# Kernel tuning notes

Hardware: AMD Instinct MI355X
Metric: run time of the kernel (lower is better)

The kernel has to match this reference:

```python
import jax, jax.numpy as jnp
import numpy as np

NEG_INF = -1e10  # masked_fill value from the torch module


def setup_inputs() -> dict:
    key = jax.random.key(0)
    k1, k2, k3, k4, k5 = jax.random.split(key, 5)
    B, S, H = 64, 2048, 512
    return {
        "decoder_hidden": jax.random.normal(k1, (B, H), dtype=jnp.float32),
        "encoder_outputs": jax.random.normal(k2, (B, S, 2 * H), dtype=jnp.float32),
        "mask": jnp.ones((B, S), dtype=jnp.int32),
        "Wd": jax.random.normal(k3, (H, H), dtype=jnp.float32) * (1.0 / np.sqrt(H)),
        "We": jax.random.normal(k4, (2 * H, H), dtype=jnp.float32) * (1.0 / np.sqrt(2 * H)),
        "v": jax.random.normal(k5, (H,), dtype=jnp.float32) * (1.0 / np.sqrt(H)),
    }


def reference(decoder_hidden, encoder_outputs, mask, Wd, We, v):
    # decoder_proj: (B, H); encoder_proj: (B, S, H)
    dec_proj = decoder_hidden @ Wd
    enc_proj = jnp.einsum("bse,eh->bsh", encoder_outputs, We)
    energy = jnp.tanh(dec_proj[:, None, :] + enc_proj)  # (B, S, H)
    scores = jnp.einsum("bsh,h->bs", energy, v)  # (B, S)
    scores = jnp.where(mask == 0, NEG_INF, scores)
    attn_weights = jax.nn.softmax(scores, axis=1)  # (B, S)
    context = jnp.einsum("bs,bsd->bd", attn_weights, encoder_outputs)  # (B, 2H)
    return (context, attn_weights)
```

## Files before the change

### kernel.cpp

```cpp
#include <hip/hip_runtime.h>

typedef _Float16 f16;
typedef f16  f16x4 __attribute__((ext_vector_type(4)));
typedef f16  f16x8 __attribute__((ext_vector_type(8)));
typedef float f32x4 __attribute__((ext_vector_type(4)));

#define B_  64
#define S_  2048
#define H_  512
#define K_  1024

__device__ __forceinline__ float fast_tanh(float x){
  float ax = fabsf(x);
  float t  = __expf(-2.0f*ax);
  float r  = (1.0f - t) / (1.0f + t);
  return x < 0.0f ? -r : r;
}

__global__ __launch_bounds__(256) void convert_we_k(const float* __restrict__ We,
                                                    f16* __restrict__ Bg){
  int idx = blockIdx.x*256 + threadIdx.x;
  int k = idx >> 9, col = idx & 511;
  Bg[((k>>3)<<12) + (col<<3) + (k&7)] = (f16)We[idx];
}

__global__ __launch_bounds__(128) void decproj_k(const float* __restrict__ dh,
                                                 const float* __restrict__ Wd,
                                                 float* __restrict__ dp){
  __shared__ float s_dh[512];
  int b = blockIdx.x >> 2, cg = blockIdx.x & 3;
  int col = (cg<<7) + threadIdx.x;
  for (int i = threadIdx.x; i < 512; i += 128) s_dh[i] = dh[(b<<9) + i];
  __syncthreads();
  float a0=0.f,a1=0.f,a2=0.f,a3=0.f;
  for (int k = 0; k < 512; k += 4){
    a0 += s_dh[k+0]*Wd[(k+0)*512 + col];
    a1 += s_dh[k+1]*Wd[(k+1)*512 + col];
    a2 += s_dh[k+2]*Wd[(k+2)*512 + col];
    a3 += s_dh[k+3]*Wd[(k+3)*512 + col];
  }
  dp[(b<<9) + col] = (a0+a1)+(a2+a3);
}

__global__ __launch_bounds__(512, 4) void scores_k(
    const float* __restrict__ enc,
    const f16*   __restrict__ Bg,
    const float* __restrict__ dp,
    const float* __restrict__ vvg,
    float*       __restrict__ scores)
{
  __shared__ __align__(16) f16 At[2][2048];
  __shared__ __align__(16) f16 Bt[2][16384];
  __shared__ float s_sc[64];

  const int tid  = threadIdx.x;
  const int lane = tid & 63;
  const int wave = tid >> 6;
  const int b    = blockIdx.x >> 5;
  const int s0   = (blockIdx.x & 31) << 6;

  if (tid < 64) s_sc[tid] = 0.0f;

  const int arow = tid >> 3;
  const int akq  = tid & 7;
  const float* aG = enc + ((size_t)(b*S_ + s0 + arow) << 10) + (akq << 2);
  const int aDst = ((akq>>1)<<9) + (arow<<3) + ((akq&1)<<2);

  const int r16 = lane & 15, g = lane >> 4;
  const int aFrag = (g<<9)  + (r16<<3);
  const int colb  = wave << 6;
  const int bFrag = (g<<12) + ((colb + r16)<<3);

  f32x4 acc[4][4] = {};

  auto stage = [&](int buf, int t){
    const f16* src = Bg + ((size_t)t << 14);
    #pragma unroll
    for (int i = 0; i < 4; ++i){
      int slot = (i<<9) + tid;
      __builtin_amdgcn_global_load_lds(
          (const __attribute__((address_space(1))) void*)(src + (slot<<3)),
          (__attribute__((address_space(3))) void*)(&Bt[buf][slot<<3]),
          16, 0, 0);
    }
    f32x4 a4 = __builtin_nontemporal_load((const f32x4*)(aG + (t<<5)));
    f16x4 h4; h4[0]=(f16)a4[0]; h4[1]=(f16)a4[1]; h4[2]=(f16)a4[2]; h4[3]=(f16)a4[3];
    *(f16x4*)&At[buf][aDst] = h4;
  };

  stage(0, 0);
  __syncthreads();

  for (int t = 0; t < 32; ++t){
    const int cur = t & 1;
    if (t < 31) stage(cur^1, t+1);
    f16x8 bfr[4];
    #pragma unroll
    for (int n = 0; n < 4; ++n) bfr[n] = *(const f16x8*)&Bt[cur][bFrag + (n<<7)];
    #pragma unroll
    for (int m = 0; m < 4; ++m){
      f16x8 af = *(const f16x8*)&At[cur][aFrag + (m<<7)];
      #pragma unroll
      for (int n = 0; n < 4; ++n)
        acc[m][n] = __builtin_amdgcn_mfma_f32_16x16x32_f16(af, bfr[n], acc[m][n], 0, 0, 0);
    }
    __syncthreads();
  }

  float dpv[4], vvv[4];
  #pragma unroll
  for (int n = 0; n < 4; ++n){
    int c = colb + (n<<4) + r16;
    dpv[n] = dp[(b<<9) + c];
    vvv[n] = vvg[c];
  }
  float sp[4][4] = {};
  #pragma unroll
  for (int m = 0; m < 4; ++m)
    #pragma unroll
    for (int n = 0; n < 4; ++n)
      #pragma unroll
      for (int r = 0; r < 4; ++r){
        float e = fast_tanh(acc[m][n][r] + dpv[n]);
        sp[m][r] += vvv[n]*e;
      }
  #pragma unroll
  for (int m = 0; m < 4; ++m)
    #pragma unroll
    for (int r = 0; r < 4; ++r){
      float x = sp[m][r];
      x += __shfl_xor(x, 1);
      x += __shfl_xor(x, 2);
      x += __shfl_xor(x, 4);
      x += __shfl_xor(x, 8);
      if (r16 == 0) atomicAdd(&s_sc[(m<<4) + (g<<2) + r], x);
    }
  __syncthreads();
  if (tid < 64) scores[((size_t)b << 11) + s0 + tid] = s_sc[tid];
}

__global__ __launch_bounds__(256) void softmax_k(const float* __restrict__ sc,
                                                 const int* __restrict__ mask,
                                                 float* __restrict__ attn){
  const int b = blockIdx.x, tid = threadIdx.x;
  const int lane = tid & 63, wv = tid >> 6;
  __shared__ float rmx[4], rsm[4];
  float vals[8];
  float mx = -3.0e38f;
  #pragma unroll
  for (int i = 0; i < 8; ++i){
    int s = tid + (i<<8);
    float x = sc[(b<<11) + s];
    if (mask[(b<<11) + s] == 0) x = -1e10f;
    vals[i] = x; mx = fmaxf(mx, x);
  }
  #pragma unroll
  for (int o = 32; o >= 1; o >>= 1) mx = fmaxf(mx, __shfl_xor(mx, o));
  if (lane == 0) rmx[wv] = mx;
  __syncthreads();
  mx = fmaxf(fmaxf(rmx[0],rmx[1]), fmaxf(rmx[2],rmx[3]));
  float sm = 0.f;
  #pragma unroll
  for (int i = 0; i < 8; ++i){ vals[i] = __expf(vals[i]-mx); sm += vals[i]; }
  #pragma unroll
  for (int o = 32; o >= 1; o >>= 1) sm += __shfl_xor(sm, o);
  if (lane == 0) rsm[wv] = sm;
  __syncthreads();
  sm = rsm[0]+rsm[1]+rsm[2]+rsm[3];
  float inv = 1.0f / sm;
  #pragma unroll
  for (int i = 0; i < 8; ++i) attn[(b<<11) + tid + (i<<8)] = vals[i]*inv;
}

__global__ __launch_bounds__(256) void ctx_partial_k(const float* __restrict__ enc,
                                                     const float* __restrict__ attn,
                                                     float* __restrict__ part){
  const int b = blockIdx.x >> 4, ch = blockIdx.x & 15;
  const int tid = threadIdx.x;
  const f32x4* e4 = (const f32x4*)(enc + ((size_t)(b*S_ + (ch<<7)) << 10)) + tid;
  const float* aw = attn + (b<<11) + (ch<<7);
  f32x4 acc = {0.f,0.f,0.f,0.f};
  #pragma unroll 4
  for (int s = 0; s < 128; ++s){
    float w = aw[s];
    f32x4 x = __builtin_nontemporal_load(e4 + s*256);
    acc += w * x;
  }
  ((f32x4*)part)[(blockIdx.x<<8) + tid] = acc;
}

__global__ __launch_bounds__(256) void ctx_reduce_k(const float* __restrict__ part,
                                                    float* __restrict__ ctx){
  const int b = blockIdx.x, tid = threadIdx.x;
  f32x4 acc = {0.f,0.f,0.f,0.f};
  #pragma unroll
  for (int c = 0; c < 16; ++c)
    acc += ((const f32x4*)part)[(((b<<4)+c)<<8) + tid];
  ((f32x4*)ctx)[(b<<8) + tid] = acc;
}

extern "C" void kernel_launch(void* const* d_in, const int* in_sizes, int n_in,
                              void* d_out, int out_size, void* d_ws, size_t ws_size,
                              hipStream_t stream){
  (void)in_sizes; (void)n_in; (void)out_size;
  const size_t WS_NEED = (1u<<20) + B_*H_*4 + B_*S_*4 + (4u<<20);
  if (ws_size < WS_NEED) return;

  const float* dec_h = (const float*)d_in[0];
  const float* enc   = (const float*)d_in[1];
  const int*   mask  = (const int*)d_in[2];
  const float* Wd    = (const float*)d_in[3];
  const float* We    = (const float*)d_in[4];
  const float* v     = (const float*)d_in[5];
  float* out  = (float*)d_out;
  float* ctx  = out;
  float* attn = out + B_*2*H_;

  f16*   Bg     = (f16*)d_ws;
  float* dproj  = (float*)((char*)d_ws + (1<<20));
  float* scores = dproj + B_*H_;
  float* part   = scores + B_*S_;

  convert_we_k <<<2048, 256, 0, stream>>>(We, Bg);
  decproj_k    <<<256, 128, 0, stream>>>(dec_h, Wd, dproj);
  scores_k     <<<2048, 512, 0, stream>>>(enc, Bg, dproj, v, scores);
  softmax_k    <<<B_, 256, 0, stream>>>(scores, mask, attn);
  ctx_partial_k<<<B_*16, 256, 0, stream>>>(enc, attn, part);
  ctx_reduce_k <<<B_, 256, 0, stream>>>(part, ctx);
}
```

Measured before the change: 323.3 us.

## Double scores tile rows, merge prep kernels, fuse softmax into context pass

The scores GEMM tile grows from 64 to 128 sequence rows per block, which halves how often the We tile is re-read per encoder row. The cost is twice the accumulators and lower occupancy (launch bounds 4 to 2). The We conversion and decoder projection now run as one launch. Softmax is folded into the context partial kernel: each block recomputes the row max and sum over the full score row and writes attn only from chunk 0. That removes a launch and an attn round trip but repeats the reduction 16 times per batch.

```diff
diff --git a/kernel.cpp b/kernel.cpp
--- a/kernel.cpp
+++ b/kernel.cpp
@@ -17,61 +17,63 @@
   return x < 0.0f ? -r : r;
 }
 
-__global__ __launch_bounds__(256) void convert_we_k(const float* __restrict__ We,
-                                                    f16* __restrict__ Bg){
-  int idx = blockIdx.x*256 + threadIdx.x;
-  int k = idx >> 9, col = idx & 511;
-  Bg[((k>>3)<<12) + (col<<3) + (k&7)] = (f16)We[idx];
-}
-
-__global__ __launch_bounds__(128) void decproj_k(const float* __restrict__ dh,
-                                                 const float* __restrict__ Wd,
-                                                 float* __restrict__ dp){
+__global__ __launch_bounds__(256) void prep_k(const float* __restrict__ We,
+                                              f16* __restrict__ Bg,
+                                              const float* __restrict__ dh,
+                                              const float* __restrict__ Wd,
+                                              float* __restrict__ dp){
   __shared__ float s_dh[512];
-  int b = blockIdx.x >> 2, cg = blockIdx.x & 3;
-  int col = (cg<<7) + threadIdx.x;
-  for (int i = threadIdx.x; i < 512; i += 128) s_dh[i] = dh[(b<<9) + i];
-  __syncthreads();
-  float a0=0.f,a1=0.f,a2=0.f,a3=0.f;
-  for (int k = 0; k < 512; k += 4){
-    a0 += s_dh[k+0]*Wd[(k+0)*512 + col];
-    a1 += s_dh[k+1]*Wd[(k+1)*512 + col];
-    a2 += s_dh[k+2]*Wd[(k+2)*512 + col];
-    a3 += s_dh[k+3]*Wd[(k+3)*512 + col];
-  }
-  dp[(b<<9) + col] = (a0+a1)+(a2+a3);
-}
-
-__global__ __launch_bounds__(512, 4) void scores_k(
+  if (blockIdx.x < 2048){
+    int idx = blockIdx.x*256 + threadIdx.x;
+    int k = idx >> 9, col = idx & 511;
+    Bg[((k>>3)<<12) + (col<<3) + (k&7)] = (f16)We[idx];
+  } else {
+    int idx = blockIdx.x - 2048;
+    int b = idx >> 1, cg = idx & 1;
+    int col = (cg<<8) + threadIdx.x;
+    for (int i = threadIdx.x; i < 512; i += 256) s_dh[i] = dh[(b<<9) + i];
+    __syncthreads();
+    float a0=0.f,a1=0.f,a2=0.f,a3=0.f;
+    for (int k = 0; k < 512; k += 4){
+      a0 += s_dh[k+0]*Wd[(k+0)*512 + col];
+      a1 += s_dh[k+1]*Wd[(k+1)*512 + col];
+      a2 += s_dh[k+2]*Wd[(k+2)*512 + col];
+      a3 += s_dh[k+3]*Wd[(k+3)*512 + col];
+    }
+    dp[(b<<9) + col] = (a0+a1)+(a2+a3);
+  }
+}
+
+__global__ __launch_bounds__(512, 2) void scores_k(
     const float* __restrict__ enc,
     const f16*   __restrict__ Bg,
     const float* __restrict__ dp,
     const float* __restrict__ vvg,
     float*       __restrict__ scores)
 {
-  __shared__ __align__(16) f16 At[2][2048];
+  __shared__ __align__(16) f16 At[2][4096];
   __shared__ __align__(16) f16 Bt[2][16384];
-  __shared__ float s_sc[64];
+  __shared__ float s_sc[128];
 
   const int tid  = threadIdx.x;
   const int lane = tid & 63;
   const int wave = tid >> 6;
-  const int b    = blockIdx.x >> 5;
-  const int s0   = (blockIdx.x & 31) << 6;
-
-  if (tid < 64) s_sc[tid] = 0.0f;
-
-  const int arow = tid >> 3;
-  const int akq  = tid & 7;
-  const float* aG = enc + ((size_t)(b*S_ + s0 + arow) << 10) + (akq << 2);
-  const int aDst = ((akq>>1)<<9) + (arow<<3) + ((akq&1)<<2);
+  const int b    = blockIdx.x >> 4;
+  const int s0   = (blockIdx.x & 15) << 7;
+
+  if (tid < 128) s_sc[tid] = 0.0f;
+
+  const int arow = tid >> 2;
+  const int akq  = tid & 3;
+  const float* aG = enc + ((size_t)(b*S_ + s0 + arow) << 10) + (akq << 3);
+  const int aDst = (akq<<10) + (arow<<3);
 
   const int r16 = lane & 15, g = lane >> 4;
-  const int aFrag = (g<<9)  + (r16<<3);
+  const int aFrag = (g<<10) + (r16<<3);
   const int colb  = wave << 6;
   const int bFrag = (g<<12) + ((colb + r16)<<3);
 
-  f32x4 acc[4][4] = {};
+  f32x4 acc[8][4] = {};
 
   auto stage = [&](int buf, int t){
     const f16* src = Bg + ((size_t)t << 14);
@@ -83,9 +85,12 @@
           (__attribute__((address_space(3))) void*)(&Bt[buf][slot<<3]),
           16, 0, 0);
     }
-    f32x4 a4 = __builtin_nontemporal_load((const f32x4*)(aG + (t<<5)));
-    f16x4 h4; h4[0]=(f16)a4[0]; h4[1]=(f16)a4[1]; h4[2]=(f16)a4[2]; h4[3]=(f16)a4[3];
-    *(f16x4*)&At[buf][aDst] = h4;
+    f32x4 a0 = __builtin_nontemporal_load((const f32x4*)(aG + (t<<5)));
+    f32x4 a1 = __builtin_nontemporal_load((const f32x4*)(aG + (t<<5) + 4));
+    f16x8 h8;
+    h8[0]=(f16)a0[0]; h8[1]=(f16)a0[1]; h8[2]=(f16)a0[2]; h8[3]=(f16)a0[3];
+    h8[4]=(f16)a1[0]; h8[5]=(f16)a1[1]; h8[6]=(f16)a1[2]; h8[7]=(f16)a1[3];
+    *(f16x8*)&At[buf][aDst] = h8;
   };
 
   stage(0, 0);
@@ -98,7 +103,7 @@
     #pragma unroll
     for (int n = 0; n < 4; ++n) bfr[n] = *(const f16x8*)&Bt[cur][bFrag + (n<<7)];
     #pragma unroll
-    for (int m = 0; m < 4; ++m){
+    for (int m = 0; m < 8; ++m){
       f16x8 af = *(const f16x8*)&At[cur][aFrag + (m<<7)];
       #pragma unroll
       for (int n = 0; n < 4; ++n)
@@ -114,9 +119,13 @@
     dpv[n] = dp[(b<<9) + c];
     vvv[n] = vvg[c];
   }
-  float sp[4][4] = {};
-  #pragma unroll
-  for (int m = 0; m < 4; ++m)
+  float sp[8][4];
+  #pragma unroll
+  for (int m = 0; m < 8; ++m)
+    #pragma unroll
+    for (int r = 0; r < 4; ++r) sp[m][r] = 0.f;
+  #pragma unroll
+  for (int m = 0; m < 8; ++m)
     #pragma unroll
     for (int n = 0; n < 4; ++n)
       #pragma unroll
@@ -125,7 +134,7 @@
         sp[m][r] += vvv[n]*e;
       }
   #pragma unroll
-  for (int m = 0; m < 4; ++m)
+  for (int m = 0; m < 8; ++m)
     #pragma unroll
     for (int r = 0; r < 4; ++r){
       float x = sp[m][r];
@@ -136,15 +145,20 @@
       if (r16 == 0) atomicAdd(&s_sc[(m<<4) + (g<<2) + r], x);
     }
   __syncthreads();
-  if (tid < 64) scores[((size_t)b << 11) + s0 + tid] = s_sc[tid];
-}
-
-__global__ __launch_bounds__(256) void softmax_k(const float* __restrict__ sc,
-                                                 const int* __restrict__ mask,
-                                                 float* __restrict__ attn){
-  const int b = blockIdx.x, tid = threadIdx.x;
+  if (tid < 128) scores[((size_t)b << 11) + s0 + tid] = s_sc[tid];
+}
+
+__global__ __launch_bounds__(256) void ctx_partial_k(const float* __restrict__ enc,
+                                                     const float* __restrict__ sc,
+                                                     const int* __restrict__ mask,
+                                                     float* __restrict__ attn,
+                                                     float* __restrict__ part){
+  const int b = blockIdx.x >> 4, ch = blockIdx.x & 15;
+  const int tid = threadIdx.x;
   const int lane = tid & 63, wv = tid >> 6;
-  __shared__ float rmx[4], rsm[4];
+  __shared__ float red[4];
+  __shared__ float s_w[128];
+
   float vals[8];
   float mx = -3.0e38f;
   #pragma unroll
@@ -156,33 +170,37 @@
   }
   #pragma unroll
   for (int o = 32; o >= 1; o >>= 1) mx = fmaxf(mx, __shfl_xor(mx, o));
-  if (lane == 0) rmx[wv] = mx;
-  __syncthreads();
-  mx = fmaxf(fmaxf(rmx[0],rmx[1]), fmaxf(rmx[2],rmx[3]));
+  if (lane == 0) red[wv] = mx;
+  __syncthreads();
+  mx = fmaxf(fmaxf(red[0],red[1]), fmaxf(red[2],red[3]));
   float sm = 0.f;
   #pragma unroll
   for (int i = 0; i < 8; ++i){ vals[i] = __expf(vals[i]-mx); sm += vals[i]; }
   #pragma unroll
   for (int o = 32; o >= 1; o >>= 1) sm += __shfl_xor(sm, o);
-  if (lane == 0) rsm[wv] = sm;
-  __syncthreads();
-  sm = rsm[0]+rsm[1]+rsm[2]+rsm[3];
+  __syncthreads();
+  if (lane == 0) red[wv] = sm;
+  __syncthreads();
+  sm = red[0]+red[1]+red[2]+red[3];
   float inv = 1.0f / sm;
-  #pragma unroll
-  for (int i = 0; i < 8; ++i) attn[(b<<11) + tid + (i<<8)] = vals[i]*inv;
-}
-
-__global__ __launch_bounds__(256) void ctx_partial_k(const float* __restrict__ enc,
-                                                     const float* __restrict__ attn,
-                                                     float* __restrict__ part){
-  const int b = blockIdx.x >> 4, ch = blockIdx.x & 15;
-  const int tid = threadIdx.x;
+
+  if (ch == 0){
+    #pragma unroll
+    for (int i = 0; i < 8; ++i) attn[(b<<11) + tid + (i<<8)] = vals[i]*inv;
+  }
+  if (tid < 128){
+    int s = (ch<<7) + tid;
+    float x = sc[(b<<11) + s];
+    if (mask[(b<<11) + s] == 0) x = -1e10f;
+    s_w[tid] = __expf(x - mx)*inv;
+  }
+  __syncthreads();
+
   const f32x4* e4 = (const f32x4*)(enc + ((size_t)(b*S_ + (ch<<7)) << 10)) + tid;
-  const float* aw = attn + (b<<11) + (ch<<7);
   f32x4 acc = {0.f,0.f,0.f,0.f};
   #pragma unroll 4
   for (int s = 0; s < 128; ++s){
-    float w = aw[s];
+    float w = s_w[s];
     f32x4 x = __builtin_nontemporal_load(e4 + s*256);
     acc += w * x;
   }
@@ -221,10 +239,8 @@
   float* scores = dproj + B_*H_;
   float* part   = scores + B_*S_;
 
-  convert_we_k <<<2048, 256, 0, stream>>>(We, Bg);
-  decproj_k    <<<256, 128, 0, stream>>>(dec_h, Wd, dproj);
-  scores_k     <<<2048, 512, 0, stream>>>(enc, Bg, dproj, v, scores);
-  softmax_k    <<<B_, 256, 0, stream>>>(scores, mask, attn);
-  ctx_partial_k<<<B_*16, 256, 0, stream>>>(enc, attn, part);
+  prep_k       <<<2176, 256, 0, stream>>>(We, Bg, dec_h, Wd, dproj);
+  scores_k     <<<1024, 512, 0, stream>>>(enc, Bg, dproj, v, scores);
+  ctx_partial_k<<<B_*16, 256, 0, stream>>>(enc, scores, mask, attn, part);
   ctx_reduce_k <<<B_, 256, 0, stream>>>(part, ctx);
 }
```

Result: slower. 372.9 us (+15.3%).

## Fuse scores, softmax numerator and context partials using a static max bound

Applied to the files above, without the earlier changes.

Replaces the separate scores, softmax and context kernels with one fused kernel. Each block exponentiates its scores against a fixed upper bound C = sum|v|, which holds because tanh is bounded, and then reuses its just-loaded encoder rows, likely still in cache, to accumulate weighted context partials. A small combine kernel then normalizes by the summed denominators. This avoids a second full pass over encoder_outputs from HBM and cuts launches. The costs are extra register pressure (launch bounds lowered to 2 waves) and possible underflow if the real scores sit far below the bound, which is guarded only by a denominator clamp.

```diff
diff --git a/kernel.cpp b/kernel.cpp
--- a/kernel.cpp
+++ b/kernel.cpp
@@ -17,37 +17,53 @@
   return x < 0.0f ? -r : r;
 }
 
-__global__ __launch_bounds__(256) void convert_we_k(const float* __restrict__ We,
-                                                    f16* __restrict__ Bg){
-  int idx = blockIdx.x*256 + threadIdx.x;
-  int k = idx >> 9, col = idx & 511;
-  Bg[((k>>3)<<12) + (col<<3) + (k&7)] = (f16)We[idx];
-}
-
-__global__ __launch_bounds__(128) void decproj_k(const float* __restrict__ dh,
-                                                 const float* __restrict__ Wd,
-                                                 float* __restrict__ dp){
+__global__ __launch_bounds__(256) void prep_k(const float* __restrict__ We,
+                                              f16* __restrict__ Bg,
+                                              const float* __restrict__ dh,
+                                              const float* __restrict__ Wd,
+                                              float* __restrict__ dp,
+                                              const float* __restrict__ vvg,
+                                              float* __restrict__ vC){
   __shared__ float s_dh[512];
-  int b = blockIdx.x >> 2, cg = blockIdx.x & 3;
-  int col = (cg<<7) + threadIdx.x;
-  for (int i = threadIdx.x; i < 512; i += 128) s_dh[i] = dh[(b<<9) + i];
-  __syncthreads();
-  float a0=0.f,a1=0.f,a2=0.f,a3=0.f;
-  for (int k = 0; k < 512; k += 4){
-    a0 += s_dh[k+0]*Wd[(k+0)*512 + col];
-    a1 += s_dh[k+1]*Wd[(k+1)*512 + col];
-    a2 += s_dh[k+2]*Wd[(k+2)*512 + col];
-    a3 += s_dh[k+3]*Wd[(k+3)*512 + col];
-  }
-  dp[(b<<9) + col] = (a0+a1)+(a2+a3);
-}
-
-__global__ __launch_bounds__(512, 4) void scores_k(
+  if (blockIdx.x < 2048){
+    int idx = blockIdx.x*256 + threadIdx.x;
+    int k = idx >> 9, col = idx & 511;
+    Bg[((k>>3)<<12) + (col<<3) + (k&7)] = (f16)We[idx];
+  } else if (blockIdx.x < 2176){
+    int idx = blockIdx.x - 2048;
+    int b = idx >> 1, cg = idx & 1;
+    int col = (cg<<8) + threadIdx.x;
+    for (int i = threadIdx.x; i < 512; i += 256) s_dh[i] = dh[(b<<9) + i];
+    __syncthreads();
+    float a0=0.f,a1=0.f,a2=0.f,a3=0.f;
+    for (int k = 0; k < 512; k += 4){
+      a0 += s_dh[k+0]*Wd[(k+0)*512 + col];
+      a1 += s_dh[k+1]*Wd[(k+1)*512 + col];
+      a2 += s_dh[k+2]*Wd[(k+2)*512 + col];
+      a3 += s_dh[k+3]*Wd[(k+3)*512 + col];
+    }
+    dp[(b<<9) + col] = (a0+a1)+(a2+a3);
+  } else {
+    int t = threadIdx.x;
+    float a = fabsf(vvg[t]) + fabsf(vvg[t+256]);
+    #pragma unroll
+    for (int o = 32; o >= 1; o >>= 1) a += __shfl_xor(a, o);
+    if ((t & 63) == 0) s_dh[t>>6] = a;
+    __syncthreads();
+    if (t == 0) vC[0] = s_dh[0]+s_dh[1]+s_dh[2]+s_dh[3];
+  }
+}
+
+__global__ __launch_bounds__(512, 2) void fused_k(
     const float* __restrict__ enc,
     const f16*   __restrict__ Bg,
     const float* __restrict__ dp,
     const float* __restrict__ vvg,
-    float*       __restrict__ scores)
+    const float* __restrict__ vC,
+    const int*   __restrict__ mask,
+    float*       __restrict__ pbuf,
+    float*       __restrict__ denom,
+    float*       __restrict__ part)
 {
   __shared__ __align__(16) f16 At[2][2048];
   __shared__ __align__(16) f16 Bt[2][16384];
@@ -83,7 +99,7 @@
           (__attribute__((address_space(3))) void*)(&Bt[buf][slot<<3]),
           16, 0, 0);
     }
-    f32x4 a4 = __builtin_nontemporal_load((const f32x4*)(aG + (t<<5)));
+    f32x4 a4 = *(const f32x4*)(aG + (t<<5));
     f16x4 h4; h4[0]=(f16)a4[0]; h4[1]=(f16)a4[1]; h4[2]=(f16)a4[2]; h4[3]=(f16)a4[3];
     *(f16x4*)&At[buf][aDst] = h4;
   };
@@ -136,74 +152,66 @@
       if (r16 == 0) atomicAdd(&s_sc[(m<<4) + (g<<2) + r], x);
     }
   __syncthreads();
-  if (tid < 64) scores[((size_t)b << 11) + s0 + tid] = s_sc[tid];
-}
-
-__global__ __launch_bounds__(256) void softmax_k(const float* __restrict__ sc,
-                                                 const int* __restrict__ mask,
+
+  const float C = vC[0];
+  if (tid < 64){
+    float s = s_sc[tid];
+    int mk = mask[(b<<11) + s0 + tid];
+    float p = mk ? __expf(s - C) : 0.0f;
+    s_sc[tid] = p;
+    pbuf[(b<<11) + s0 + tid] = p;
+    float d = p;
+    #pragma unroll
+    for (int o = 32; o >= 1; o >>= 1) d += __shfl_xor(d, o);
+    if (tid == 0) denom[(b<<5) + (blockIdx.x & 31)] = d;
+  }
+  __syncthreads();
+
+  {
+    const float2* e2 = (const float2*)(enc + ((size_t)(b*S_ + s0) << 10)) + tid;
+    float ax = 0.f, ay = 0.f;
+    #pragma unroll 4
+    for (int s = 0; s < 64; ++s){
+      float w = s_sc[s];
+      float2 x = e2[s*512];
+      ax += w * x.x; ay += w * x.y;
+    }
+    float2* pp = (float2*)part + ((size_t)blockIdx.x << 9) + tid;
+    *pp = make_float2(ax, ay);
+  }
+}
+
+__global__ __launch_bounds__(256) void combine_k(const float* __restrict__ part,
+                                                 const float* __restrict__ denom,
+                                                 const float* __restrict__ pbuf,
+                                                 float* __restrict__ ctx,
                                                  float* __restrict__ attn){
   const int b = blockIdx.x, tid = threadIdx.x;
-  const int lane = tid & 63, wv = tid >> 6;
-  __shared__ float rmx[4], rsm[4];
-  float vals[8];
-  float mx = -3.0e38f;
+  float D = 0.f;
+  #pragma unroll
+  for (int c = 0; c < 32; ++c) D += denom[(b<<5) + c];
+  D = fmaxf(D, 1e-37f);
+  const float inv = 1.0f / D;
+
+  f32x4 acc = {0.f,0.f,0.f,0.f};
+  const f32x4* p4 = (const f32x4*)part;
+  #pragma unroll
+  for (int c = 0; c < 32; ++c)
+    acc += p4[(((b<<5)+c)<<8) + tid];
+  ((f32x4*)ctx)[(b<<8) + tid] = acc * inv;
+
   #pragma unroll
   for (int i = 0; i < 8; ++i){
     int s = tid + (i<<8);
-    float x = sc[(b<<11) + s];
-    if (mask[(b<<11) + s] == 0) x = -1e10f;
-    vals[i] = x; mx = fmaxf(mx, x);
-  }
-  #pragma unroll
-  for (int o = 32; o >= 1; o >>= 1) mx = fmaxf(mx, __shfl_xor(mx, o));
-  if (lane == 0) rmx[wv] = mx;
-  __syncthreads();
-  mx = fmaxf(fmaxf(rmx[0],rmx[1]), fmaxf(rmx[2],rmx[3]));
-  float sm = 0.f;
-  #pragma unroll
-  for (int i = 0; i < 8; ++i){ vals[i] = __expf(vals[i]-mx); sm += vals[i]; }
-  #pragma unroll
-  for (int o = 32; o >= 1; o >>= 1) sm += __shfl_xor(sm, o);
-  if (lane == 0) rsm[wv] = sm;
-  __syncthreads();
-  sm = rsm[0]+rsm[1]+rsm[2]+rsm[3];
-  float inv = 1.0f / sm;
-  #pragma unroll
-  for (int i = 0; i < 8; ++i) attn[(b<<11) + tid + (i<<8)] = vals[i]*inv;
-}
-
-__global__ __launch_bounds__(256) void ctx_partial_k(const float* __restrict__ enc,
-                                                     const float* __restrict__ attn,
-                                                     float* __restrict__ part){
-  const int b = blockIdx.x >> 4, ch = blockIdx.x & 15;
-  const int tid = threadIdx.x;
-  const f32x4* e4 = (const f32x4*)(enc + ((size_t)(b*S_ + (ch<<7)) << 10)) + tid;
-  const float* aw = attn + (b<<11) + (ch<<7);
-  f32x4 acc = {0.f,0.f,0.f,0.f};
-  #pragma unroll 4
-  for (int s = 0; s < 128; ++s){
-    float w = aw[s];
-    f32x4 x = __builtin_nontemporal_load(e4 + s*256);
-    acc += w * x;
-  }
-  ((f32x4*)part)[(blockIdx.x<<8) + tid] = acc;
-}
-
-__global__ __launch_bounds__(256) void ctx_reduce_k(const float* __restrict__ part,
-                                                    float* __restrict__ ctx){
-  const int b = blockIdx.x, tid = threadIdx.x;
-  f32x4 acc = {0.f,0.f,0.f,0.f};
-  #pragma unroll
-  for (int c = 0; c < 16; ++c)
-    acc += ((const f32x4*)part)[(((b<<4)+c)<<8) + tid];
-  ((f32x4*)ctx)[(b<<8) + tid] = acc;
+    attn[(b<<11) + s] = pbuf[(b<<11) + s] * inv;
+  }
 }
 
 extern "C" void kernel_launch(void* const* d_in, const int* in_sizes, int n_in,
                               void* d_out, int out_size, void* d_ws, size_t ws_size,
                               hipStream_t stream){
   (void)in_sizes; (void)n_in; (void)out_size;
-  const size_t WS_NEED = (1u<<20) + B_*H_*4 + B_*S_*4 + (4u<<20);
+  const size_t WS_NEED = 1712384u + 8388608u;
   if (ws_size < WS_NEED) return;
 
   const float* dec_h = (const float*)d_in[0];
@@ -216,15 +224,15 @@
   float* ctx  = out;
   float* attn = out + B_*2*H_;
 
-  f16*   Bg     = (f16*)d_ws;
-  float* dproj  = (float*)((char*)d_ws + (1<<20));
-  float* scores = dproj + B_*H_;
-  float* part   = scores + B_*S_;
-
-  convert_we_k <<<2048, 256, 0, stream>>>(We, Bg);
-  decproj_k    <<<256, 128, 0, stream>>>(dec_h, Wd, dproj);
-  scores_k     <<<2048, 512, 0, stream>>>(enc, Bg, dproj, v, scores);
-  softmax_k    <<<B_, 256, 0, stream>>>(scores, mask, attn);
-  ctx_partial_k<<<B_*16, 256, 0, stream>>>(enc, attn, part);
-  ctx_reduce_k <<<B_, 256, 0, stream>>>(part, ctx);
-}
+  char* ws = (char*)d_ws;
+  f16*   Bg     = (f16*)ws;
+  float* dproj  = (float*)(ws + 1048576);
+  float* vC     = (float*)(ws + 1179648);
+  float* pbuf   = (float*)(ws + 1179904);
+  float* denom  = (float*)(ws + 1704192);
+  float* part   = (float*)(ws + 1712384);
+
+  prep_k   <<<2177, 256, 0, stream>>>(We, Bg, dec_h, Wd, dproj, v, vC);
+  fused_k  <<<2048, 512, 0, stream>>>(enc, Bg, dproj, v, vC, mask, pbuf, denom, part);
+  combine_k<<<B_, 256, 0, stream>>>(part, denom, pbuf, ctx, attn);
+}
```

Result: faster. 296.8 us (-8.2%).
